# Kernel optimization log

Hardware: AMD Instinct MI355X
Metric: run time of the kernel (lower is better)

## Reference

```python
import jax, jax.numpy as jnp
import numpy as np
from jax import lax

NT = 100
NUM_LEVELS = 9

_KERNEL = jnp.array([[0.0, 0.25, 0.0],
                     [0.25, 0.0, 0.25],
                     [0.0, 0.25, 0.0]], dtype=jnp.float32).reshape(1, 1, 3, 3)


def _conv(x):
    # 3x3 Jacobi stencil, padding=1 (SAME), NCHW layout
    return lax.conv_general_dilated(x, _KERNEL.astype(x.dtype), (1, 1), 'SAME',
                                    dimension_numbers=('NCHW', 'OIHW', 'NCHW'))


def _avg_pool2(x):
    n, c, h, w = x.shape
    return x.reshape(n, c, h // 2, 2, w // 2, 2).mean(axis=(3, 5))


def _interp(x, th, tw):
    n, c = x.shape[:2]
    # bilinear, align_corners=False (half-pixel centers) == jax.image bilinear
    return jax.image.resize(x, (n, c, th, tw), method='bilinear')


def _jacobi(x, mask, nt):
    def step(x, _):
        x_next = _conv(x)
        return x_next * mask + x * (1 - mask), None
    x, _ = lax.scan(step, x, None, length=nt)
    return x


def setup_inputs() -> dict:
    key = jax.random.key(0)
    ks = jax.random.split(key, 12)
    inp = {'X': jax.random.normal(ks[0], (1, 1, 1024, 1024), dtype=jnp.float32)}
    sizes = [1024, 512, 256, 128, 64, 32, 16, 8, 4, 4]
    for i, s in enumerate(sizes):
        inp[f'Mask{i + 1}'] = jax.random.uniform(ks[i + 1], (1, 1, s, s), dtype=jnp.float32)
    return inp


def reference(X, Mask1, Mask2, Mask3, Mask4, Mask5, Mask6, Mask7, Mask8, Mask9, Mask10):
    masks = [Mask1, Mask2, Mask3, Mask4, Mask5, Mask6, Mask7, Mask8, Mask9, Mask10]
    grids = [X]
    # Restriction sweep: fine -> coarse
    for level in range(1, NUM_LEVELS):
        g = grids[level - 1]
        m = masks[level - 1]
        masked_out = _conv(g * (m > 0).astype(g.dtype))
        unmasked_out = _conv(g * (1 - m))
        residual = masked_out + unmasked_out
        grids.append(_avg_pool2(residual))
    # Coarse solve: Jacobi relaxation on coarsest grid with Mask9
    grids[-1] = _jacobi(grids[-1], Mask9, NT)
    # Prolongation sweep: coarse -> fine
    for level in range(NUM_LEVELS - 2, -1, -1):
        th, tw = grids[level].shape[-2:]
        fine = _interp(grids[level + 1], th, tw) + grids[level]
        m = masks[level]
        fine = _conv(fine * (m > 0).astype(fine.dtype)) + _conv(fine * (1 - m))
        grids[level + 1] = fine  # mirror torch list mutation semantics loosely
    # torch code pops down to grids[0] (original X) and runs fine Jacobi on it
    final_solution = grids[0]
    final_solution = _jacobi(final_solution, Mask1, NT)
    return final_solution
```

## Files before the change

### kernel.cpp

```cpp
#include <hip/hip_runtime.h>


#define W 1024
#define H 1024
#define TILE_W 128
#define TILE_H 64
#define TI 10
#define OS_X 104
#define OS_Y 44
#define HX 12
#define NBX 10
#define NBY 24
#define NLAUNCH 10

typedef unsigned uint2v __attribute__((ext_vector_type(2)));

__device__ __forceinline__ float4 ld4(const float* __restrict__ p, int gr, int gc) {
    if ((unsigned)gr < (unsigned)H && (unsigned)gc < (unsigned)W)
        return *(const float4*)&p[gr * W + gc];
    return make_float4(0.f, 0.f, 0.f, 0.f);
}

__device__ __forceinline__ float4 rowstep(const float4 up, const float4 ce,
                                          const float4 dn, const float lf,
                                          const float rt, const float4 m) {
    float4 s, n;
    s.x = (up.x + dn.x) + (lf   + ce.y);
    s.y = (up.y + dn.y) + (ce.x + ce.z);
    s.z = (up.z + dn.z) + (ce.y + ce.w);
    s.w = (up.w + dn.w) + (ce.z + rt);
    n.x = fmaf(m.x, fmaf(0.25f, s.x, -ce.x), ce.x);
    n.y = fmaf(m.y, fmaf(0.25f, s.y, -ce.y), ce.y);
    n.z = fmaf(m.z, fmaf(0.25f, s.z, -ce.z), ce.z);
    n.w = fmaf(m.w, fmaf(0.25f, s.w, -ce.w), ce.w);
    return n;
}

__device__ __forceinline__ float xchg32(float p) {
    unsigned u = __float_as_uint(p);
    uint2v r = __builtin_amdgcn_permlane32_swap(u, u, false, false);
    return __uint_as_float(r.x ^ r.y ^ u);
}

__device__ __forceinline__ float4 xchg32_4(const float4 p) {
    return make_float4(xchg32(p.x), xchg32(p.y), xchg32(p.z), xchg32(p.w));
}

__device__ __forceinline__ float4 sel4(bool c, const float4 a, const float4 b) {
    return make_float4(c ? a.x : b.x, c ? a.y : b.y,
                       c ? a.z : b.z, c ? a.w : b.w);
}

__global__ __launch_bounds__(512, 1) void jacobi_trap(
    const float* __restrict__ xin, const float* __restrict__ mask,
    float* __restrict__ xout)
{
    __shared__ float4 SLs[2][18][34];
    __shared__ float4 SRs[2][18][34];
    __shared__ float4 STs[2][10][32];
    __shared__ float4 SBs[2][10][32];

    const int tid = threadIdx.x;
    const int pr  = tid >> 5;
    const int pc  = tid & 31;
    const int wid = tid >> 6;
    const bool lowHalf = (tid & 32) == 0;
    const int gx0 = (int)blockIdx.x * OS_X - HX;
    const int gy0 = (int)blockIdx.y * OS_Y - TI;
    const int gr0 = gy0 + pr * 4;
    const int gc0 = gx0 + pc * 4;

    float4 c[4], m[4];
    #pragma unroll
    for (int i = 0; i < 4; ++i) {
        c[i] = ld4(xin,  gr0 + i, gc0);
        m[i] = ld4(mask, gr0 + i, gc0);
    }

    const float4 z4 = make_float4(0.f, 0.f, 0.f, 0.f);
    if (tid < 72) {
        int b = tid / 36, r2 = tid % 36;
        if (r2 < 18) SRs[b][r2][0] = z4;
        else         SLs[b][r2 - 18][33] = z4;
    } else if (tid >= 128 && tid < 256) {
        int j = tid - 128, b = j >> 6, r3 = j & 63;
        if (r3 < 32) STs[b][9][r3] = z4;
        else         SBs[b][0][r3 - 32] = z4;
    }

    SLs[0][pr + 1][pc + 1] = make_float4(c[0].x, c[1].x, c[2].x, c[3].x);
    SRs[0][pr + 1][pc + 1] = make_float4(c[0].w, c[1].w, c[2].w, c[3].w);
    if (lowHalf) STs[0][wid + 1][pc] = c[0];
    else         SBs[0][wid + 1][pc] = c[3];
    __syncthreads();

    #pragma unroll 1
    for (int it = 0; it < TI; ++it) {
        const int rb = it & 1;

        const float4 p4 = sel4(lowHalf, c[3], c[0]);
        const float4 q4 = xchg32_4(p4);

        float4 thL = z4, bhL = z4;
        if (lowHalf) thL = SBs[rb][wid][pc];
        else         bhL = STs[rb][wid + 2][pc];
        const float4 th = sel4(lowHalf, thL, q4);
        const float4 bh = sel4(lowHalf, q4, bhL);

        const float4 lh = SRs[rb][pr + 1][pc];
        const float4 rh = SLs[rb][pr + 1][pc + 2];

        const float4 n0 = rowstep(th,   c[0], c[1], lh.x, rh.x, m[0]);
        const float4 n1 = rowstep(c[0], c[1], c[2], lh.y, rh.y, m[1]);
        const float4 n2 = rowstep(c[1], c[2], c[3], lh.z, rh.z, m[2]);
        const float4 n3 = rowstep(c[2], c[3], bh,   lh.w, rh.w, m[3]);
        c[0] = n0; c[1] = n1; c[2] = n2; c[3] = n3;

        if (it < TI - 1) {
            const int wb = rb ^ 1;
            SLs[wb][pr + 1][pc + 1] = make_float4(n0.x, n1.x, n2.x, n3.x);
            SRs[wb][pr + 1][pc + 1] = make_float4(n0.w, n1.w, n2.w, n3.w);
            if (lowHalf) STs[wb][wid + 1][pc] = n0;
            else         SBs[wb][wid + 1][pc] = n3;
            __syncthreads();
        }
    }

    const int lc = pc * 4;
    if (lc >= HX && lc < HX + OS_X && (unsigned)gc0 < (unsigned)W) {
        #pragma unroll
        for (int i = 0; i < 4; ++i) {
            int lr = pr * 4 + i;
            if (lr < TI || lr >= TILE_H - TI) continue;
            int gr = gy0 + lr;
            if ((unsigned)gr >= (unsigned)H) continue;
            *(float4*)&xout[gr * W + gc0] = c[i];
        }
    }
}

extern "C" void kernel_launch(void* const* d_in, const int* in_sizes, int n_in,
                              void* d_out, int out_size, void* d_ws, size_t ws_size,
                              hipStream_t stream) {
    const float* X = (const float*)d_in[0];
    const float* M = (const float*)d_in[1];
    float* out = (float*)d_out;
    float* ws  = (float*)d_ws;

    dim3 grid(NBX, NBY), block(512);
    const float* src = X;
    for (int l = 0; l < NLAUNCH; ++l) {
        float* dst = (l & 1) ? out : ws;
        jacobi_trap<<<grid, block, 0, stream>>>(src, M, dst);
        src = dst;
    }
}
```

Before: 102.8 us.

## Deepen temporal blocking to 20 steps per launch with six rows per thread

Each launch now advances 20 Jacobi steps instead of 10, with taller 128x96 tiles, wider halos, six rows per thread and extra float2 shared-memory side buffers. This halves the number of kernel launches and global-memory round trips, and gives each thread more independent work between barriers. In exchange, the larger halo means more redundant computation per useful output point and higher register pressure per thread. The ping-pong buffer choice is adjusted so the last launch still writes to the output.

```diff
diff --git a/kernel.cpp b/kernel.cpp
--- a/kernel.cpp
+++ b/kernel.cpp
@@ -4,14 +4,14 @@
 #define W 1024
 #define H 1024
 #define TILE_W 128
-#define TILE_H 64
-#define TI 10
-#define OS_X 104
-#define OS_Y 44
-#define HX 12
-#define NBX 10
-#define NBY 24
-#define NLAUNCH 10
+#define TILE_H 96
+#define TI 20
+#define OS_X 88
+#define OS_Y 56
+#define HX 20
+#define NBX 12
+#define NBY 19
+#define NLAUNCH 5
 
 typedef unsigned uint2v __attribute__((ext_vector_type(2)));
 
@@ -55,8 +55,10 @@
     const float* __restrict__ xin, const float* __restrict__ mask,
     float* __restrict__ xout)
 {
-    __shared__ float4 SLs[2][18][34];
-    __shared__ float4 SRs[2][18][34];
+    __shared__ float4 SL4[2][18][34];
+    __shared__ float4 SR4[2][18][34];
+    __shared__ float2 SL2[2][18][34];
+    __shared__ float2 SR2[2][18][34];
     __shared__ float4 STs[2][10][32];
     __shared__ float4 SBs[2][10][32];
 
@@ -67,38 +69,45 @@
     const bool lowHalf = (tid & 32) == 0;
     const int gx0 = (int)blockIdx.x * OS_X - HX;
     const int gy0 = (int)blockIdx.y * OS_Y - TI;
-    const int gr0 = gy0 + pr * 4;
+    const int gr0 = gy0 + pr * 6;
     const int gc0 = gx0 + pc * 4;
 
-    float4 c[4], m[4];
+    float4 c[6], m[6];
     #pragma unroll
-    for (int i = 0; i < 4; ++i) {
+    for (int i = 0; i < 6; ++i) {
         c[i] = ld4(xin,  gr0 + i, gc0);
         m[i] = ld4(mask, gr0 + i, gc0);
     }
 
     const float4 z4 = make_float4(0.f, 0.f, 0.f, 0.f);
+    const float2 z2 = make_float2(0.f, 0.f);
     if (tid < 72) {
         int b = tid / 36, r2 = tid % 36;
-        if (r2 < 18) SRs[b][r2][0] = z4;
-        else         SLs[b][r2 - 18][33] = z4;
-    } else if (tid >= 128 && tid < 256) {
-        int j = tid - 128, b = j >> 6, r3 = j & 63;
-        if (r3 < 32) STs[b][9][r3] = z4;
-        else         SBs[b][0][r3 - 32] = z4;
+        if (r2 < 18) SR4[b][r2][0] = z4;
+        else         SL4[b][r2 - 18][33] = z4;
+    } else if (tid < 144) {
+        int j = tid - 72, b = j / 36, r2 = j % 36;
+        if (r2 < 18) SR2[b][r2][0] = z2;
+        else         SL2[b][r2 - 18][33] = z2;
+    } else if (tid < 272) {
+        int j = tid - 144, b = j >> 6, rem = j & 63;
+        if (rem < 32) STs[b][9][rem] = z4;
+        else          SBs[b][0][rem - 32] = z4;
     }
 
-    SLs[0][pr + 1][pc + 1] = make_float4(c[0].x, c[1].x, c[2].x, c[3].x);
-    SRs[0][pr + 1][pc + 1] = make_float4(c[0].w, c[1].w, c[2].w, c[3].w);
+    SL4[0][pr + 1][pc + 1] = make_float4(c[0].x, c[1].x, c[2].x, c[3].x);
+    SL2[0][pr + 1][pc + 1] = make_float2(c[4].x, c[5].x);
+    SR4[0][pr + 1][pc + 1] = make_float4(c[0].w, c[1].w, c[2].w, c[3].w);
+    SR2[0][pr + 1][pc + 1] = make_float2(c[4].w, c[5].w);
     if (lowHalf) STs[0][wid + 1][pc] = c[0];
-    else         SBs[0][wid + 1][pc] = c[3];
+    else         SBs[0][wid + 1][pc] = c[5];
     __syncthreads();
 
     #pragma unroll 1
     for (int it = 0; it < TI; ++it) {
         const int rb = it & 1;
 
-        const float4 p4 = sel4(lowHalf, c[3], c[0]);
+        const float4 p4 = sel4(lowHalf, c[5], c[0]);
         const float4 q4 = xchg32_4(p4);
 
         float4 thL = z4, bhL = z4;
@@ -107,30 +116,35 @@
         const float4 th = sel4(lowHalf, thL, q4);
         const float4 bh = sel4(lowHalf, q4, bhL);
 
-        const float4 lh = SRs[rb][pr + 1][pc];
-        const float4 rh = SLs[rb][pr + 1][pc + 2];
+        const float4 lh4 = SR4[rb][pr + 1][pc];
+        const float2 lh2 = SR2[rb][pr + 1][pc];
+        const float4 rh4 = SL4[rb][pr + 1][pc + 2];
+        const float2 rh2 = SL2[rb][pr + 1][pc + 2];
 
-        const float4 n0 = rowstep(th,   c[0], c[1], lh.x, rh.x, m[0]);
-        const float4 n1 = rowstep(c[0], c[1], c[2], lh.y, rh.y, m[1]);
-        const float4 n2 = rowstep(c[1], c[2], c[3], lh.z, rh.z, m[2]);
-        const float4 n3 = rowstep(c[2], c[3], bh,   lh.w, rh.w, m[3]);
-        c[0] = n0; c[1] = n1; c[2] = n2; c[3] = n3;
+        const float4 n0 = rowstep(th,   c[0], c[1], lh4.x, rh4.x, m[0]);
+        const float4 n1 = rowstep(c[0], c[1], c[2], lh4.y, rh4.y, m[1]);
+        const float4 n2 = rowstep(c[1], c[2], c[3], lh4.z, rh4.z, m[2]);
+        const float4 n3 = rowstep(c[2], c[3], c[4], lh4.w, rh4.w, m[3]);
+        const float4 n4 = rowstep(c[3], c[4], c[5], lh2.x, rh2.x, m[4]);
+        const float4 n5 = rowstep(c[4], c[5], bh,   lh2.y, rh2.y, m[5]);
+        c[0] = n0; c[1] = n1; c[2] = n2; c[3] = n3; c[4] = n4; c[5] = n5;
 
         if (it < TI - 1) {
             const int wb = rb ^ 1;
-            SLs[wb][pr + 1][pc + 1] = make_float4(n0.x, n1.x, n2.x, n3.x);
-            SRs[wb][pr + 1][pc + 1] = make_float4(n0.w, n1.w, n2.w, n3.w);
+            SL4[wb][pr + 1][pc + 1] = make_float4(n0.x, n1.x, n2.x, n3.x);
+            SL2[wb][pr + 1][pc + 1] = make_float2(n4.x, n5.x);
+            SR4[wb][pr + 1][pc + 1] = make_float4(n0.w, n1.w, n2.w, n3.w);
+            SR2[wb][pr + 1][pc + 1] = make_float2(n4.w, n5.w);
             if (lowHalf) STs[wb][wid + 1][pc] = n0;
-            else         SBs[wb][wid + 1][pc] = n3;
+            else         SBs[wb][wid + 1][pc] = n5;
             __syncthreads();
         }
     }
 
-    const int lc = pc * 4;
-    if (lc >= HX && lc < HX + OS_X && (unsigned)gc0 < (unsigned)W) {
+    if (pc >= 5 && pc <= 26 && (unsigned)gc0 < (unsigned)W) {
         #pragma unroll
-        for (int i = 0; i < 4; ++i) {
-            int lr = pr * 4 + i;
+        for (int i = 0; i < 6; ++i) {
+            int lr = pr * 6 + i;
             if (lr < TI || lr >= TILE_H - TI) continue;
             int gr = gy0 + lr;
             if ((unsigned)gr >= (unsigned)H) continue;
@@ -150,7 +164,7 @@
     dim3 grid(NBX, NBY), block(512);
     const float* src = X;
     for (int l = 0; l < NLAUNCH; ++l) {
-        float* dst = (l & 1) ? out : ws;
+        float* dst = ((NLAUNCH - 1 - l) & 1) ? ws : out;
         jacobi_trap<<<grid, block, 0, stream>>>(src, M, dst);
         src = dst;
     }
```

After: 102.8 us. No clear change (-0.0%).
